# Performance work log

Hardware: AMD Instinct MI355X
Metric: run time of the kernel (lower is better)

Reference implementation:

```python
import jax, jax.numpy as jnp
import numpy as np

N = 50000      # nodes
E = 800000     # edges (avg degree 16)
F_IN = 512
HID = 128
OUT = 40


def setup_inputs() -> dict:
    key = jax.random.key(0)
    ks = jax.random.split(key, 6)
    x = jax.random.normal(ks[0], (N, F_IN), dtype=jnp.float32)
    edge_index = jax.random.randint(ks[1], (2, E), 0, N, dtype=jnp.int64)
    edge_weight = jax.random.uniform(ks[2], (E,), dtype=jnp.float32)
    # Glorot-ish init for the two GCNConv weight matrices
    W1 = jax.random.normal(ks[3], (F_IN, HID), dtype=jnp.float32) * (1.0 / np.sqrt(F_IN))
    b1 = jnp.zeros((HID,), dtype=jnp.float32)
    W2 = jax.random.normal(ks[4], (HID, OUT), dtype=jnp.float32) * (1.0 / np.sqrt(HID))
    b2 = jnp.zeros((OUT,), dtype=jnp.float32)
    return {"x": x, "edge_index": edge_index, "edge_weight": edge_weight,
            "W1": W1, "b1": b1, "W2": W2, "b2": b2}


def gcn_layer(x, edge_index, edge_weight, W, b):
    """PyG GCNConv (normalize=True, add_self_loops=True):
    out = D^{-1/2} (A + I) D^{-1/2} (x @ W) + b, with weighted edges."""
    n = x.shape[0]
    h = x @ W  # [n, F_out] dense transform before aggregation
    sl = jnp.arange(n)
    row = jnp.concatenate([edge_index[0], sl])   # source nodes
    col = jnp.concatenate([edge_index[1], sl])   # target nodes
    w = jnp.concatenate([edge_weight, jnp.ones((n,), x.dtype)])  # self-loop weight 1
    deg = jax.ops.segment_sum(w, col, num_segments=n)            # in-degree (weighted)
    dinv = jnp.where(deg > 0, jax.lax.rsqrt(deg), 0.0)
    norm = dinv[row] * w * dinv[col]                             # per-edge coefficient
    # gather-source, scale, scatter-add into target
    out = jax.ops.segment_sum(h[row] * norm[:, None], col, num_segments=n)
    return out + b


def reference(x, edge_index, edge_weight, W1, b1, W2, b2):
    h = jax.nn.relu(gcn_layer(x, edge_index, edge_weight, W1, b1))
    # dropout is identity at inference (training=False)
    h = gcn_layer(h, edge_index, edge_weight, W2, b2)
    return jax.nn.log_softmax(h, axis=1)
```

## Files before the change

kernel.cpp:

```cpp
#include <hip/hip_runtime.h>
#include <math.h>

#define N_NODES 50000
#define F_IN    512
#define HID     128
#define OUT_C   40
#define NPAD    48
#define E_EDGES 800000
#define LDA 40
#define LDK 136
#define MAXDEG 64
#define ESTRIDE 40
#define G1B 391
#define DEGB 3125

typedef __attribute__((ext_vector_type(8))) short short8;
typedef __attribute__((ext_vector_type(4))) float f32x4;
typedef __attribute__((ext_vector_type(4))) unsigned uint4v;

__device__ __forceinline__ unsigned short f2bf(float f) {
    union { float f; unsigned u; } v; v.f = f;
    unsigned u = v.u + 0x7fffu + ((v.u >> 16) & 1u);
    return (unsigned short)(u >> 16);
}
__device__ __forceinline__ float bflo(unsigned u) { return __uint_as_float(u << 16); }
__device__ __forceinline__ float bfhi(unsigned u) { return __uint_as_float(u & 0xffff0000u); }
__device__ __forceinline__ unsigned cvtpk(float lo, float hi) {
    unsigned r;
    asm("v_cvt_pk_bf16_f32 %0, %1, %2" : "=v"(r) : "v"(lo), "v"(hi));
    return r;
}
__device__ __forceinline__ float pk2dinv(unsigned long long pk) {
    return rsqrtf(1.0f + (float)(pk & 0xFFFFFFFFFFULL) * (1.0f / 4294967296.0f));
}


__global__ __launch_bounds__(256) void k_initwprep(const float* __restrict__ W1,
                                                   const float* __restrict__ W2,
                                                   unsigned short* __restrict__ W1bt,
                                                   unsigned short* __restrict__ W2bt,
                                                   unsigned long long* __restrict__ packed) {
    int idx = blockIdx.x * 256 + threadIdx.x;
    if (idx < N_NODES) packed[idx] = 0ULL;
    if (idx < F_IN * HID) {
        int k = idx & 511, n = idx >> 9;
        W1bt[(size_t)n * F_IN + k] = f2bf(W1[(size_t)k * HID + n]);
    } else if (idx < F_IN * HID + NPAD * HID) {
        int i2 = idx - F_IN * HID;
        int k = i2 & 127, n = i2 >> 7;
        W2bt[n * HID + k] = (n < OUT_C) ? f2bf(W2[(size_t)k * OUT_C + n]) : 0;
    }
}


__global__ __launch_bounds__(256) void k_g1deg(const float* __restrict__ X,
                                               const unsigned short* __restrict__ W1bt,
                                               unsigned short* __restrict__ Hb,
                                               const int* __restrict__ row,
                                               const int* __restrict__ col,
                                               const float* __restrict__ ew,
                                               unsigned long long* __restrict__ packed,
                                               unsigned* __restrict__ es) {
    const int tid = threadIdx.x;
    if (blockIdx.x >= G1B) {
        int e = (blockIdx.x - G1B) * 256 + tid;
        if (e < E_EDGES) {
            int c   = col[e];
            int r   = row[e];
            float w = ew[e];
            unsigned long long fx = (unsigned long long)(w * 4294967296.0f);
            unsigned long long old = atomicAdd(&packed[c], (1ULL << 40) | fx);
            int rk = (int)(old >> 40);
            if (rk < ESTRIDE)
                es[(size_t)c * ESTRIDE + rk] = (unsigned)r | ((unsigned)f2bf(w) << 16);
        }
        return;
    }

    __shared__ __align__(16) unsigned short As[128 * LDA];
    __shared__ __align__(16) unsigned short Bs[128 * LDA];
    const int row0 = blockIdx.x * 128;
    const int lane = tid & 63;
    const int w    = tid >> 6;
    const int quad = lane >> 4;
    const int l16  = lane & 15;
    const int wm   = (w >> 1) * 64;
    const int wn   = (w & 1) * 64;

    f32x4 acc[4][4] = {};

    const int sr = tid >> 1;
    const int kg = (tid & 1) * 16;
    int arow = row0 + sr;
    if (arow >= N_NODES) arow = N_NODES - 1;
    const float*          xp = X + (size_t)arow * F_IN + kg;
    const unsigned short* bp = W1bt + (size_t)sr * F_IN + kg;
    unsigned short* asw = &As[sr * LDA + kg];
    unsigned short* bsw = &Bs[sr * LDA + kg];

    float4 xa = *(const float4*)(xp);
    float4 xb = *(const float4*)(xp + 4);
    float4 xc = *(const float4*)(xp + 8);
    float4 xd = *(const float4*)(xp + 12);
    short8 wa = *(const short8*)(bp);
    short8 wb = *(const short8*)(bp + 8);

    for (int k0 = 0; k0 < F_IN; k0 += 32) {
        uint4v pa, pb;
        pa[0] = cvtpk(xa.x, xa.y); pa[1] = cvtpk(xa.z, xa.w);
        pa[2] = cvtpk(xb.x, xb.y); pa[3] = cvtpk(xb.z, xb.w);
        pb[0] = cvtpk(xc.x, xc.y); pb[1] = cvtpk(xc.z, xc.w);
        pb[2] = cvtpk(xd.x, xd.y); pb[3] = cvtpk(xd.z, xd.w);
        short8 cwa = wa, cwb = wb;

        if (k0 + 32 < F_IN) {
            xa = *(const float4*)(xp + k0 + 32);
            xb = *(const float4*)(xp + k0 + 36);
            xc = *(const float4*)(xp + k0 + 40);
            xd = *(const float4*)(xp + k0 + 44);
            wa = *(const short8*)(bp + k0 + 32);
            wb = *(const short8*)(bp + k0 + 40);
        }

        *(uint4v*)(asw)      = pa;
        *(uint4v*)(asw + 8)  = pb;
        *(short8*)(bsw)      = cwa;
        *(short8*)(bsw + 8)  = cwb;
        asm volatile("s_waitcnt lgkmcnt(0)" ::: "memory");
        __builtin_amdgcn_s_barrier();
        asm volatile("" ::: "memory");

        short8 af[4], bf[4];
#pragma unroll
        for (int i = 0; i < 4; i++)
            af[i] = *(const short8*)&As[(wm + i * 16 + l16) * LDA + quad * 8];
#pragma unroll
        for (int j = 0; j < 4; j++)
            bf[j] = *(const short8*)&Bs[(wn + j * 16 + l16) * LDA + quad * 8];
#pragma unroll
        for (int i = 0; i < 4; i++)
#pragma unroll
            for (int j = 0; j < 4; j++)
                acc[i][j] = __builtin_amdgcn_mfma_f32_16x16x32_bf16(
                    af[i], bf[j], acc[i][j], 0, 0, 0);
        asm volatile("" ::: "memory");
        __builtin_amdgcn_s_barrier();
        asm volatile("" ::: "memory");
    }

#pragma unroll
    for (int i = 0; i < 4; i++) {
#pragma unroll
        for (int r = 0; r < 4; r++) {
            int grow = row0 + wm + i * 16 + quad * 4 + r;
            if (grow < N_NODES) {
#pragma unroll
                for (int j = 0; j < 4; j++) {
                    int gcol = wn + j * 16 + l16;
                    Hb[(size_t)grow * HID + gcol] = f2bf(acc[i][j][r]);
                }
            }
        }
    }
}


__global__ __launch_bounds__(256) void k_agg1(const unsigned long long* __restrict__ packed,
                                              const unsigned* __restrict__ es,
                                              const unsigned short* __restrict__ H1b,
                                              const float* __restrict__ b1,
                                              unsigned short* __restrict__ A1b) {
    __shared__ int2 sE[4][MAXDEG];
    const int tid  = threadIdx.x;
    const int wv   = tid >> 6;
    const int lane = tid & 63;
    const int node = blockIdx.x * 4 + wv;
    if (node >= N_NODES) return;
    const int h = lane >> 5;
    const int l = lane & 31;

    const unsigned long long pkn = packed[node];
    const int   d  = (int)(pkn >> 40);
    const float di = pk2dinv(pkn);
    const size_t base = (size_t)node * ESTRIDE;
    int dl = (d < ESTRIDE) ? d : ESTRIDE;
    const int dp = (dl + 15) & ~15;
    for (int p = lane; p < dp; p += 64) {
        int2 t = make_int2(0, 0);
        if (p < dl) {
            unsigned u = es[base + p];
            float dv = pk2dinv(packed[u & 0xffffu]);
            t.x = (int)(u & 0xffffu);
            t.y = __float_as_int(bfhi(u) * dv);
        }
        sE[wv][p] = t;
    }

    const uint2 sv = *(const uint2*)&H1b[(size_t)node * HID + l * 4];
    float a0, a1, a2, a3;
    if (h == 0) {
        a0 = di * bflo(sv.x); a1 = di * bfhi(sv.x);
        a2 = di * bflo(sv.y); a3 = di * bfhi(sv.y);
    } else {
        a0 = a1 = a2 = a3 = 0.0f;
    }

    for (int p = 0; p < dp; p += 16) {
        const int bs = p + h * 8;
        int s_[8]; float n_[8];
#pragma unroll
        for (int j = 0; j < 8; j++) {
            int2 t = sE[wv][bs + j];
            s_[j] = t.x; n_[j] = __int_as_float(t.y);
        }
        uint2 g[8];
#pragma unroll
        for (int j = 0; j < 8; j++)
            g[j] = *(const uint2*)&H1b[(size_t)s_[j] * HID + l * 4];
#pragma unroll
        for (int j = 0; j < 8; j++) {
            a0 = fmaf(bflo(g[j].x), n_[j], a0);
            a1 = fmaf(bfhi(g[j].x), n_[j], a1);
            a2 = fmaf(bflo(g[j].y), n_[j], a2);
            a3 = fmaf(bfhi(g[j].y), n_[j], a3);
        }
    }

    a0 += __shfl_xor(a0, 32);
    a1 += __shfl_xor(a1, 32);
    a2 += __shfl_xor(a2, 32);
    a3 += __shfl_xor(a3, 32);

    if (h == 0) {
        const float4 bv = *(const float4*)&b1[l * 4];
        float r0 = fmaxf(fmaf(di, a0, bv.x), 0.0f);
        float r1 = fmaxf(fmaf(di, a1, bv.y), 0.0f);
        float r2 = fmaxf(fmaf(di, a2, bv.z), 0.0f);
        float r3 = fmaxf(fmaf(di, a3, bv.w), 0.0f);
        uint2 pk;
        pk.x = cvtpk(r0, r1);
        pk.y = cvtpk(r2, r3);
        *(uint2*)&A1b[(size_t)node * HID + l * 4] = pk;
    }
}


__global__ __launch_bounds__(256) void k_gemm2_mfma(const unsigned short* __restrict__ A1b,
                                                    const unsigned short* __restrict__ W2bt,
                                                    const unsigned long long* __restrict__ packed,
                                                    unsigned short* __restrict__ H2b) {
    __shared__ __align__(16) unsigned short As[128 * LDK];
    __shared__ __align__(16) unsigned short Bs[NPAD * LDK];
    const int tid  = threadIdx.x;
    const int row0 = blockIdx.x * 128;
    const int lane = tid & 63;
    const int w    = tid >> 6;
    const int quad = lane >> 4;
    const int l16  = lane & 15;

#pragma unroll
    for (int i = 0; i < 8; i++) {
        int id = tid + i * 256;
        int r = id >> 4, kc = (id & 15) * 8;
        int ar = row0 + r; if (ar >= N_NODES) ar = N_NODES - 1;
        *(short8*)&As[r * LDK + kc] = *(const short8*)&A1b[(size_t)ar * HID + kc];
    }
#pragma unroll
    for (int i = 0; i < 3; i++) {
        int id = tid + i * 256;
        int n = id >> 4, kc = (id & 15) * 8;
        *(short8*)&Bs[n * LDK + kc] = *(const short8*)&W2bt[n * HID + kc];
    }
    __syncthreads();

    f32x4 acc[2][3] = {};
    const int rbase = w * 32;
#pragma unroll
    for (int ks = 0; ks < 4; ks++) {
        const int k0 = ks * 32 + quad * 8;
        short8 af[2], bf[3];
#pragma unroll
        for (int i = 0; i < 2; i++)
            af[i] = *(const short8*)&As[(rbase + i * 16 + l16) * LDK + k0];
#pragma unroll
        for (int j = 0; j < 3; j++)
            bf[j] = *(const short8*)&Bs[(j * 16 + l16) * LDK + k0];
#pragma unroll
        for (int i = 0; i < 2; i++)
#pragma unroll
            for (int j = 0; j < 3; j++)
                acc[i][j] = __builtin_amdgcn_mfma_f32_16x16x32_bf16(
                    af[i], bf[j], acc[i][j], 0, 0, 0);
    }

#pragma unroll
    for (int i = 0; i < 2; i++) {
#pragma unroll
        for (int r = 0; r < 4; r++) {
            int grow = row0 + rbase + i * 16 + quad * 4 + r;
            if (grow < N_NODES) {
                float dv = pk2dinv(packed[grow]);
#pragma unroll
                for (int j = 0; j < 3; j++)
                    H2b[(size_t)grow * NPAD + j * 16 + l16] = f2bf(dv * acc[i][j][r]);
            }
        }
    }
}


__global__ __launch_bounds__(256) void k_agg2_lsm(const unsigned long long* __restrict__ packed,
                                                  const unsigned* __restrict__ es,
                                                  const unsigned short* __restrict__ H2b,
                                                  const float* __restrict__ b2,
                                                  float* __restrict__ out) {
    __shared__ int2 sE[4][MAXDEG];
    const int tid  = threadIdx.x;
    const int wv   = tid >> 6;
    const int lane = tid & 63;
    const int node = blockIdx.x * 4 + wv;
    if (node >= N_NODES) return;
    const int h = lane >> 5;
    const int l = lane & 31;
    const bool act = (l < 20);

    const unsigned long long pkn = packed[node];
    const int   d  = (int)(pkn >> 40);
    const float di = pk2dinv(pkn);
    const size_t base = (size_t)node * ESTRIDE;
    int dl = (d < ESTRIDE) ? d : ESTRIDE;
    const int dp = (dl + 15) & ~15;
    for (int p = lane; p < dp; p += 64) {
        int2 t = make_int2(0, 0);
        if (p < dl) {
            unsigned u = es[base + p];
            t.x = (int)(u & 0xffffu);
            t.y = __float_as_int(bfhi(u));
        }
        sE[wv][p] = t;
    }

    float a0 = 0.0f, a1 = 0.0f;
    if (h == 0 && act) {
        unsigned sv = *(const unsigned*)&H2b[(size_t)node * NPAD + 2 * l];
        a0 = bflo(sv); a1 = bfhi(sv);
    }

    for (int p = 0; p < dp; p += 16) {
        const int bs = p + h * 8;
        int s_[8]; float n_[8];
#pragma unroll
        for (int j = 0; j < 8; j++) {
            int2 t = sE[wv][bs + j];
            s_[j] = t.x; n_[j] = __int_as_float(t.y);
        }
        if (act) {
            unsigned g[8];
#pragma unroll
            for (int j = 0; j < 8; j++)
                g[j] = *(const unsigned*)&H2b[(size_t)s_[j] * NPAD + 2 * l];
#pragma unroll
            for (int j = 0; j < 8; j++) {
                a0 = fmaf(bflo(g[j]), n_[j], a0);
                a1 = fmaf(bfhi(g[j]), n_[j], a1);
            }
        }
    }

    a0 += __shfl_xor(a0, 32);
    a1 += __shfl_xor(a1, 32);

    float v0 = 0.0f, v1 = 0.0f;
    if (act) {
        float2 bv = *(const float2*)&b2[2 * l];
        v0 = fmaf(di, a0, bv.x);
        v1 = fmaf(di, a1, bv.y);
    }

    float m = act ? fmaxf(v0, v1) : -INFINITY;
#pragma unroll
    for (int off = 16; off > 0; off >>= 1) m = fmaxf(m, __shfl_xor(m, off));
    float ex = act ? (__expf(v0 - m) + __expf(v1 - m)) : 0.0f;
    float s = ex;
#pragma unroll
    for (int off = 16; off > 0; off >>= 1) s += __shfl_xor(s, off);
    if (h == 0 && act) {
        float lg = __logf(s);
        *(float2*)&out[(size_t)node * OUT_C + 2 * l] =
            make_float2(v0 - m - lg, v1 - m - lg);
    }
}


extern "C" void kernel_launch(void* const* d_in, const int* in_sizes, int n_in,
                              void* d_out, int out_size, void* d_ws, size_t ws_size,
                              hipStream_t stream) {
    const float* x  = (const float*)d_in[0];
    const int*   ei = (const int*)d_in[1];
    const float* ew = (const float*)d_in[2];
    const float* W1 = (const float*)d_in[3];
    const float* b1 = (const float*)d_in[4];
    const float* W2 = (const float*)d_in[5];
    const float* b2 = (const float*)d_in[6];
    float* out = (float*)d_out;

    const int* row = ei;
    const int* col = ei + E_EDGES;

    float* ws = (float*)d_ws;
    unsigned long long* packed = (unsigned long long*)ws;
    unsigned short* H1b  = (unsigned short*)(ws + 100000);
    unsigned short* H2b  = (unsigned short*)(ws + 100000);
    unsigned short* A1b  = (unsigned short*)(ws + 3300000);
    unsigned short* W1bt = (unsigned short*)(ws + 6500000);
    unsigned short* W2bt = (unsigned short*)(ws + 6532768);
    unsigned* es         = (unsigned*)(ws + 6535840);

    const int B = 256;

    k_initwprep<<<(F_IN * HID + NPAD * HID + B - 1) / B, B, 0, stream>>>(
        W1, W2, W1bt, W2bt, packed);

    k_g1deg<<<G1B + DEGB, B, 0, stream>>>(x, W1bt, H1b, row, col, ew, packed, es);

    k_agg1<<<(N_NODES + 3) / 4, B, 0, stream>>>(packed, es, H1b, b1, A1b);

    k_gemm2_mfma<<<(N_NODES + 127) / 128, B, 0, stream>>>(A1b, W2bt, packed, H2b);

    k_agg2_lsm<<<(N_NODES + 3) / 4, B, 0, stream>>>(packed, es, H2b, b2, out);
}
```

Measured before the change: 260.5 us.

## Pack degree counter into 32-bit atomics and widen agg1 gathers to 16 bytes

The per-node degree/count accumulator shrinks from a 64-bit word (24-bit count, 40-bit fixed-point weight) to a 32-bit word (6-bit count, 26-bit fixed-point weight with 20 fractional bits). This halves atomic and read traffic on the packed array and uses cheaper 32-bit atomics. It lowers weighted-degree precision and overflows the count field for nodes with in-degree of 64 or more. Separately, agg1 now has each lane load 8 bf16 values (uint4) over 4 edge groups with a two-step shuffle reduction, instead of 4 values over 2 groups, giving wider memory transactions per gather.

```diff
diff --git a/kernel.cpp b/kernel.cpp
--- a/kernel.cpp
+++ b/kernel.cpp
@@ -30,8 +30,8 @@
     asm("v_cvt_pk_bf16_f32 %0, %1, %2" : "=v"(r) : "v"(lo), "v"(hi));
     return r;
 }
-__device__ __forceinline__ float pk2dinv(unsigned long long pk) {
-    return rsqrtf(1.0f + (float)(pk & 0xFFFFFFFFFFULL) * (1.0f / 4294967296.0f));
+__device__ __forceinline__ float pk2dinv(unsigned pk) {
+    return rsqrtf(1.0f + (float)(pk & 0x03FFFFFFu) * (1.0f / 1048576.0f));
 }
 
 
@@ -39,9 +39,9 @@
                                                    const float* __restrict__ W2,
                                                    unsigned short* __restrict__ W1bt,
                                                    unsigned short* __restrict__ W2bt,
-                                                   unsigned long long* __restrict__ packed) {
+                                                   unsigned* __restrict__ packed) {
     int idx = blockIdx.x * 256 + threadIdx.x;
-    if (idx < N_NODES) packed[idx] = 0ULL;
+    if (idx < N_NODES) packed[idx] = 0u;
     if (idx < F_IN * HID) {
         int k = idx & 511, n = idx >> 9;
         W1bt[(size_t)n * F_IN + k] = f2bf(W1[(size_t)k * HID + n]);
@@ -59,7 +59,7 @@
                                                const int* __restrict__ row,
                                                const int* __restrict__ col,
                                                const float* __restrict__ ew,
-                                               unsigned long long* __restrict__ packed,
+                                               unsigned* __restrict__ packed,
                                                unsigned* __restrict__ es) {
     const int tid = threadIdx.x;
     if (blockIdx.x >= G1B) {
@@ -68,9 +68,9 @@
             int c   = col[e];
             int r   = row[e];
             float w = ew[e];
-            unsigned long long fx = (unsigned long long)(w * 4294967296.0f);
-            unsigned long long old = atomicAdd(&packed[c], (1ULL << 40) | fx);
-            int rk = (int)(old >> 40);
+            unsigned fx = (unsigned)(w * 1048576.0f);
+            unsigned old = atomicAdd(&packed[c], (1u << 26) | fx);
+            int rk = (int)(old >> 26);
             if (rk < ESTRIDE)
                 es[(size_t)c * ESTRIDE + rk] = (unsigned)r | ((unsigned)f2bf(w) << 16);
         }
@@ -165,7 +165,7 @@
 }
 
 
-__global__ __launch_bounds__(256) void k_agg1(const unsigned long long* __restrict__ packed,
+__global__ __launch_bounds__(256) void k_agg1(const unsigned* __restrict__ packed,
                                               const unsigned* __restrict__ es,
                                               const unsigned short* __restrict__ H1b,
                                               const float* __restrict__ b1,
@@ -176,11 +176,11 @@
     const int lane = tid & 63;
     const int node = blockIdx.x * 4 + wv;
     if (node >= N_NODES) return;
-    const int h = lane >> 5;
-    const int l = lane & 31;
-
-    const unsigned long long pkn = packed[node];
-    const int   d  = (int)(pkn >> 40);
+    const int q   = lane >> 4;
+    const int l16 = lane & 15;
+
+    const unsigned pkn = packed[node];
+    const int   d  = (int)(pkn >> 26);
     const float di = pk2dinv(pkn);
     const size_t base = (size_t)node * ESTRIDE;
     int dl = (d < ESTRIDE) ? d : ESTRIDE;
@@ -196,58 +196,73 @@
         sE[wv][p] = t;
     }
 
-    const uint2 sv = *(const uint2*)&H1b[(size_t)node * HID + l * 4];
-    float a0, a1, a2, a3;
-    if (h == 0) {
-        a0 = di * bflo(sv.x); a1 = di * bfhi(sv.x);
-        a2 = di * bflo(sv.y); a3 = di * bfhi(sv.y);
+    const uint4 sv = *(const uint4*)&H1b[(size_t)node * HID + l16 * 8];
+    float a[8];
+    if (q == 0) {
+        a[0] = di * bflo(sv.x); a[1] = di * bfhi(sv.x);
+        a[2] = di * bflo(sv.y); a[3] = di * bfhi(sv.y);
+        a[4] = di * bflo(sv.z); a[5] = di * bfhi(sv.z);
+        a[6] = di * bflo(sv.w); a[7] = di * bfhi(sv.w);
     } else {
-        a0 = a1 = a2 = a3 = 0.0f;
+#pragma unroll
+        for (int k = 0; k < 8; k++) a[k] = 0.0f;
     }
 
     for (int p = 0; p < dp; p += 16) {
-        const int bs = p + h * 8;
-        int s_[8]; float n_[8];
-#pragma unroll
-        for (int j = 0; j < 8; j++) {
+        const int bs = p + q * 4;
+        int s_[4]; float n_[4];
+#pragma unroll
+        for (int j = 0; j < 4; j++) {
             int2 t = sE[wv][bs + j];
             s_[j] = t.x; n_[j] = __int_as_float(t.y);
         }
-        uint2 g[8];
-#pragma unroll
-        for (int j = 0; j < 8; j++)
-            g[j] = *(const uint2*)&H1b[(size_t)s_[j] * HID + l * 4];
-#pragma unroll
-        for (int j = 0; j < 8; j++) {
-            a0 = fmaf(bflo(g[j].x), n_[j], a0);
-            a1 = fmaf(bfhi(g[j].x), n_[j], a1);
-            a2 = fmaf(bflo(g[j].y), n_[j], a2);
-            a3 = fmaf(bfhi(g[j].y), n_[j], a3);
-        }
-    }
-
-    a0 += __shfl_xor(a0, 32);
-    a1 += __shfl_xor(a1, 32);
-    a2 += __shfl_xor(a2, 32);
-    a3 += __shfl_xor(a3, 32);
-
-    if (h == 0) {
-        const float4 bv = *(const float4*)&b1[l * 4];
-        float r0 = fmaxf(fmaf(di, a0, bv.x), 0.0f);
-        float r1 = fmaxf(fmaf(di, a1, bv.y), 0.0f);
-        float r2 = fmaxf(fmaf(di, a2, bv.z), 0.0f);
-        float r3 = fmaxf(fmaf(di, a3, bv.w), 0.0f);
-        uint2 pk;
-        pk.x = cvtpk(r0, r1);
-        pk.y = cvtpk(r2, r3);
-        *(uint2*)&A1b[(size_t)node * HID + l * 4] = pk;
+        uint4 g[4];
+#pragma unroll
+        for (int j = 0; j < 4; j++)
+            g[j] = *(const uint4*)&H1b[(size_t)s_[j] * HID + l16 * 8];
+#pragma unroll
+        for (int j = 0; j < 4; j++) {
+            a[0] = fmaf(bflo(g[j].x), n_[j], a[0]);
+            a[1] = fmaf(bfhi(g[j].x), n_[j], a[1]);
+            a[2] = fmaf(bflo(g[j].y), n_[j], a[2]);
+            a[3] = fmaf(bfhi(g[j].y), n_[j], a[3]);
+            a[4] = fmaf(bflo(g[j].z), n_[j], a[4]);
+            a[5] = fmaf(bfhi(g[j].z), n_[j], a[5]);
+            a[6] = fmaf(bflo(g[j].w), n_[j], a[6]);
+            a[7] = fmaf(bfhi(g[j].w), n_[j], a[7]);
+        }
+    }
+
+#pragma unroll
+    for (int k = 0; k < 8; k++) {
+        a[k] += __shfl_xor(a[k], 16);
+        a[k] += __shfl_xor(a[k], 32);
+    }
+
+    if (q == 0) {
+        const float4 bv0 = *(const float4*)&b1[l16 * 8];
+        const float4 bv1 = *(const float4*)&b1[l16 * 8 + 4];
+        float r0 = fmaxf(fmaf(di, a[0], bv0.x), 0.0f);
+        float r1 = fmaxf(fmaf(di, a[1], bv0.y), 0.0f);
+        float r2 = fmaxf(fmaf(di, a[2], bv0.z), 0.0f);
+        float r3 = fmaxf(fmaf(di, a[3], bv0.w), 0.0f);
+        float r4 = fmaxf(fmaf(di, a[4], bv1.x), 0.0f);
+        float r5 = fmaxf(fmaf(di, a[5], bv1.y), 0.0f);
+        float r6 = fmaxf(fmaf(di, a[6], bv1.z), 0.0f);
+        float r7 = fmaxf(fmaf(di, a[7], bv1.w), 0.0f);
+        uint4 pk4;
+        pk4.x = cvtpk(r0, r1);
+        pk4.y = cvtpk(r2, r3);
+        pk4.z = cvtpk(r4, r5);
+        pk4.w = cvtpk(r6, r7);
+        *(uint4*)&A1b[(size_t)node * HID + l16 * 8] = pk4;
     }
 }
 
 
 __global__ __launch_bounds__(256) void k_gemm2_mfma(const unsigned short* __restrict__ A1b,
                                                     const unsigned short* __restrict__ W2bt,
-                                                    const unsigned long long* __restrict__ packed,
+                                                    const unsigned* __restrict__ packed,
                                                     unsigned short* __restrict__ H2b) {
     __shared__ __align__(16) unsigned short As[128 * LDK];
     __shared__ __align__(16) unsigned short Bs[NPAD * LDK];
@@ -309,7 +324,7 @@
 }
 
 
-__global__ __launch_bounds__(256) void k_agg2_lsm(const unsigned long long* __restrict__ packed,
+__global__ __launch_bounds__(256) void k_agg2_lsm(const unsigned* __restrict__ packed,
                                                   const unsigned* __restrict__ es,
                                                   const unsigned short* __restrict__ H2b,
                                                   const float* __restrict__ b2,
@@ -324,8 +339,8 @@
     const int l = lane & 31;
     const bool act = (l < 20);
 
-    const unsigned long long pkn = packed[node];
-    const int   d  = (int)(pkn >> 40);
+    const unsigned pkn = packed[node];
+    const int   d  = (int)(pkn >> 26);
     const float di = pk2dinv(pkn);
     const size_t base = (size_t)node * ESTRIDE;
     int dl = (d < ESTRIDE) ? d : ESTRIDE;
@@ -408,7 +423,7 @@
     const int* col = ei + E_EDGES;
 
     float* ws = (float*)d_ws;
-    unsigned long long* packed = (unsigned long long*)ws;
+    unsigned* packed     = (unsigned*)ws;
     unsigned short* H1b  = (unsigned short*)(ws + 100000);
     unsigned short* H2b  = (unsigned short*)(ws + 100000);
     unsigned short* A1b  = (unsigned short*)(ws + 3300000);
```

Result: no change. 257.1 us, median of 3 (-1.3%).
